# Performance work log

Measured on AMD Instinct MI355X. Metric: run time of the kernel, lower is better.

Reference implementation:

```python
import jax, jax.numpy as jnp
import numpy as np

B, S, H = 2, 2048, 2048
NH, NKV, HD = 16, 4, 128
NEG = -1e9


def rotate_half(x):
    x1, x2 = x[..., : x.shape[-1] // 2], x[..., x.shape[-1] // 2 :]
    return jnp.concatenate((-x2, x1), axis=-1)


def setup_inputs() -> dict:
    key = jax.random.key(0)
    ks = jax.random.split(key, 6)
    hidden_states = jax.random.normal(ks[0], (B, S, H), dtype=jnp.float32)
    # causal additive mask [B, 1, S, S]
    causal = jnp.tril(jnp.ones((S, S), dtype=bool))
    attention_mask = jnp.where(causal, 0.0, NEG).astype(jnp.float32)
    attention_mask = jnp.broadcast_to(attention_mask, (B, 1, S, S))
    # rotary embeddings, base 10000
    inv_freq = 1.0 / (10000.0 ** (np.arange(0, HD, 2, dtype=np.float32) / HD))
    pos = np.arange(S, dtype=np.float32)
    freqs = np.outer(pos, inv_freq)  # [S, HD/2]
    emb = np.concatenate([freqs, freqs], axis=-1)  # [S, HD]
    cos = jnp.broadcast_to(jnp.asarray(np.cos(emb)), (B, S, HD))
    sin = jnp.broadcast_to(jnp.asarray(np.sin(emb)), (B, S, HD))
    sc = 0.02
    Wq = jax.random.normal(ks[1], (H, NH * HD), dtype=jnp.float32) * sc
    Wk = jax.random.normal(ks[2], (H, NKV * HD), dtype=jnp.float32) * sc
    Wv = jax.random.normal(ks[3], (H, NKV * HD), dtype=jnp.float32) * sc
    Wo = jax.random.normal(ks[4], (H, H), dtype=jnp.float32) * sc
    return {"hidden_states": hidden_states, "attention_mask": attention_mask,
            "cos": cos, "sin": sin, "Wq": Wq, "Wk": Wk, "Wv": Wv, "Wo": Wo}


def reference(hidden_states, attention_mask, cos, sin, Wq, Wk, Wv, Wo):
    b, s, _ = hidden_states.shape
    # projections -> [b, heads, s, hd]
    q = (hidden_states @ Wq).reshape(b, s, NH, HD).transpose(0, 2, 1, 3)
    k = (hidden_states @ Wk).reshape(b, s, NKV, HD).transpose(0, 2, 1, 3)
    v = (hidden_states @ Wv).reshape(b, s, NKV, HD).transpose(0, 2, 1, 3)
    # RoPE (cos/sin unsqueezed at dim 1)
    c, sn = cos[:, None], sin[:, None]
    q = q * c + rotate_half(q) * sn
    k = k * c + rotate_half(k) * sn
    # GQA repeat_kv: [b, nkv, s, hd] -> [b, nh, s, hd]
    n_rep = NH // NKV
    k = jnp.repeat(k, n_rep, axis=1)
    v = jnp.repeat(v, n_rep, axis=1)
    scores = jnp.einsum("bhqd,bhkd->bhqk", q, k) / jnp.sqrt(jnp.float32(HD))
    scores = scores + attention_mask
    probs = jax.nn.softmax(scores.astype(jnp.float32), axis=-1).astype(q.dtype)
    out = jnp.einsum("bhqk,bhkd->bhqd", probs, v)
    out = out.transpose(0, 2, 1, 3).reshape(b, s, NH * HD)
    return out @ Wo
```

## Files before the change

### kernel.cpp

```cpp
#include <hip/hip_runtime.h>
#include <hip/hip_bf16.h>

typedef __bf16 bf16;
typedef __bf16 bf16x4 __attribute__((ext_vector_type(4)));
typedef __bf16 bf16x8 __attribute__((ext_vector_type(8)));
typedef float f32x4 __attribute__((ext_vector_type(4)));

__device__ __forceinline__ void gload_lds16(const void* g, void* l) {
  __builtin_amdgcn_global_load_lds((__attribute__((address_space(1))) void*)(g),
                                   (__attribute__((address_space(3))) void*)(l), 16, 0, 0);
}
__device__ __forceinline__ float fexp2(float x) {
  float r;
  asm volatile("v_exp_f32 %0, %1" : "=v"(r) : "v"(x));
  return r;
}

__global__ void k_diag(float* __restrict__ o, float v) { o[threadIdx.x] = v; }

__global__ void k_cvt_bf16(const float* __restrict__ x, bf16* __restrict__ y, int n4) {
  int i = blockIdx.x * blockDim.x + threadIdx.x;
  if (i < n4) {
    float4 v = reinterpret_cast<const float4*>(x)[i];
    bf16x4 o = {(bf16)v.x, (bf16)v.y, (bf16)v.z, (bf16)v.w};
    reinterpret_cast<bf16x4*>(y)[i] = o;
  }
}

__global__ void k_transpose_w(const float* __restrict__ W, bf16* __restrict__ Wt, int K, int N) {
  __shared__ float tile[32][33];
  int kb = blockIdx.x * 32, nb = blockIdx.y * 32;
  int tx = threadIdx.x & 31, ty = threadIdx.x >> 5;
#pragma unroll
  for (int i = 0; i < 32; i += 8)
    tile[ty + i][tx] = W[(size_t)(kb + ty + i) * N + nb + tx];
  __syncthreads();
#pragma unroll
  for (int i = 0; i < 32; i += 8)
    Wt[(size_t)(nb + ty + i) * K + kb + tx] = (bf16)tile[tx][ty + i];
}

__global__ void k_transpose_v(const bf16* __restrict__ KVb, bf16* __restrict__ Vt) {
  __shared__ bf16 tile[32][34];
  constexpr int S = 2048;
  int sb = blockIdx.x * 32, db = blockIdx.y * 32, bh = blockIdx.z;
  int b = bh >> 2, kvh = bh & 3;
  int tx = threadIdx.x & 31, ty = threadIdx.x >> 5;
  const bf16* src = KVb + (size_t)b * S * 1024 + 512 + kvh * 128;
#pragma unroll
  for (int i = 0; i < 32; i += 8)
    tile[ty + i][tx] = src[(size_t)(sb + ty + i) * 1024 + db + tx];
  __syncthreads();
  bf16* dst = Vt + (size_t)bh * 128 * S;
#pragma unroll
  for (int i = 0; i < 32; i += 8)
    dst[(size_t)(db + ty + i) * S + sb + tx] = tile[tx][ty + i];
}

template <typename OT>
__global__ __launch_bounds__(256) void k_gemm(const bf16* __restrict__ A, const bf16* __restrict__ Bt,
                                              OT* __restrict__ C, int M, int N, int Kd) {
  __shared__ __align__(16) bf16 sA[2][128 * 32];
  __shared__ __align__(16) bf16 sB[2][128 * 32];
  const int t = threadIdx.x;
  const int w = t >> 6, l = t & 63;
  const int lr = l & 15, lk = l >> 4;
  const int gx = gridDim.x, nwg = gx * gridDim.y;
  const int flat = blockIdx.y * gx + blockIdx.x;
  const int vid = (flat & 7) * (nwg >> 3) + (flat >> 3);
  const int m0 = (vid % gx) * 128, n0 = (vid / gx) * 128;
  const int wm = (w >> 1) * 64, wn = (w & 1) * 64;
  const bf16* ga = A + (size_t)(m0 + (t >> 2)) * Kd + (t & 3) * 8;
  const bf16* gb = Bt + (size_t)(n0 + (t >> 2)) * Kd + (t & 3) * 8;
  const size_t rowskip = (size_t)64 * Kd;
  auto stage = [&](int k0, int buf) {
    gload_lds16(ga + k0, sA[buf] + w * 512);
    gload_lds16(ga + rowskip + k0, sA[buf] + w * 512 + 2048);
    gload_lds16(gb + k0, sB[buf] + w * 512);
    gload_lds16(gb + rowskip + k0, sB[buf] + w * 512 + 2048);
  };
  f32x4 acc[4][4] = {};
  stage(0, 0);
  __syncthreads();
  int cur = 0;
  for (int k0 = 0; k0 < Kd; k0 += 32) {
    if (k0 + 32 < Kd) stage(k0 + 32, cur ^ 1);
    bf16x8 af[4], bfr[4];
#pragma unroll
    for (int i = 0; i < 4; ++i)
      af[i] = *reinterpret_cast<const bf16x8*>(sA[cur] + (wm + i * 16 + lr) * 32 + lk * 8);
#pragma unroll
    for (int j = 0; j < 4; ++j)
      bfr[j] = *reinterpret_cast<const bf16x8*>(sB[cur] + (wn + j * 16 + lr) * 32 + lk * 8);
#pragma unroll
    for (int i = 0; i < 4; ++i)
#pragma unroll
      for (int j = 0; j < 4; ++j)
        acc[i][j] = __builtin_amdgcn_mfma_f32_16x16x32_bf16(af[i], bfr[j], acc[i][j], 0, 0, 0);
    __syncthreads();
    cur ^= 1;
  }
#pragma unroll
  for (int i = 0; i < 4; ++i)
#pragma unroll
    for (int j = 0; j < 4; ++j)
#pragma unroll
      for (int r = 0; r < 4; ++r) {
        int row = m0 + wm + i * 16 + lk * 4 + r;
        int col = n0 + wn + j * 16 + lr;
        if constexpr (sizeof(OT) == 4)
          C[(size_t)row * N + col] = acc[i][j][r];
        else
          C[(size_t)row * N + col] = (bf16)acc[i][j][r];
      }
}

__global__ void k_rope(bf16* __restrict__ X, const float* __restrict__ cs, const float* __restrict__ sn,
                       int nh, int rowstride, float scale, int total) {
  int idx = blockIdx.x * blockDim.x + threadIdx.x;
  if (idx >= total) return;
  int d = idx & 63;
  int th = idx >> 6;
  int h = th % nh;
  int tok = th / nh;
  size_t base = (size_t)tok * rowstride + h * 128;
  float c = cs[tok * 128 + d], s = sn[tok * 128 + d];
  float x1 = (float)X[base + d];
  float x2 = (float)X[base + d + 64];
  X[base + d] = (bf16)((x1 * c - x2 * s) * scale);
  X[base + d + 64] = (bf16)((x2 * c + x1 * s) * scale);
}

__global__ __launch_bounds__(256) void k_attn(const bf16* __restrict__ Q, const bf16* __restrict__ KV,
                                              const bf16* __restrict__ Vt, bf16* __restrict__ O) {
  constexpr int S = 2048, NH = 16, HD = 128, QSTR = NH * HD, KVSTR = 1024;
  __shared__ __align__(16) bf16 sK[2][64 * 128];
  __shared__ __align__(16) bf16 sV[2][128 * 64];
  __shared__ __align__(16) bf16 sP[4][16][72];
  const int bid = blockIdx.x;
  const int vid = (bid & 7) * 64 + (bid >> 3);
  const int p = vid & 15, bh = vid >> 4;
  const int h = bh & 15, b = bh >> 4;
  const int t = threadIdx.x, w = t >> 6, l = t & 63;
  const int lr = l & 15, lk = l >> 4;
  const int kvh = h >> 2;
  const int swz = (lr & 7) << 4;

  const char* kbase = (const char*)(KV + (size_t)b * S * KVSTR + kvh * HD);
  const int krow_l = w * 16 + (l >> 4);
  const int kcol_l = (l & 15) << 4;
  const char* vtbase = (const char*)(Vt + (size_t)(b * 4 + kvh) * HD * S);
  const int vrow_l = w * 32 + (l >> 3);
  const int vcol_l = (l & 7) << 4;
  char* sKb = (char*)sK;
  char* sVb = (char*)sV;
  auto stage = [&](int kvb, int buf) {
#pragma unroll
    for (int c = 0; c < 4; ++c) {
      const int krow = krow_l + c * 4;
      gload_lds16(kbase + (size_t)(kvb + krow) * 2048 + (kcol_l ^ ((krow & 7) << 4)),
                  sKb + buf * 16384 + (w * 4 + c) * 1024);
      const int vrow = vrow_l + c * 8;
      gload_lds16(vtbase + (size_t)vrow * (S * 2) + kvb * 2 + (vcol_l ^ ((vrow & 7) << 4)),
                  sVb + buf * 16384 + (w * 4 + c) * 1024);
    }
  };

  for (int seg = 0; seg < 2; ++seg) {
    const int qtl = seg ? (31 - p) : p;
    const int qw = qtl * 64 + w * 16;
    const int ntiles = qtl + 1;
    int cur = 0;
    stage(0, 0);
    const bf16* Qp = Q + (size_t)(b * S + qw + lr) * QSTR + h * HD + lk * 8;
    bf16x8 qf[4];
#pragma unroll
    for (int i = 0; i < 4; ++i) qf[i] = *reinterpret_cast<const bf16x8*>(Qp + i * 32);
    f32x4 oacc[8] = {};
    float mrow[4] = {-3e38f, -3e38f, -3e38f, -3e38f};
    float lsum[4] = {0.f, 0.f, 0.f, 0.f};
    __syncthreads();
    for (int tt = 0; tt < ntiles; ++tt) {
      const int kvb = tt * 64;
      if (tt + 1 < ntiles) stage(kvb + 64, cur ^ 1);
      const char* sKc = sKb + cur * 16384;
      const char* sVc = sVb + cur * 16384;
      float pm[4][4];
#pragma unroll
      for (int c = 0; c < 4; ++c) {
        f32x4 s4 = {};
#pragma unroll
        for (int kf = 0; kf < 4; ++kf) {
          bf16x8 kf8 = *reinterpret_cast<const bf16x8*>(
              sKc + (c * 16 + lr) * 256 + (((kf * 64) + (lk << 4)) ^ swz));
          s4 = __builtin_amdgcn_mfma_f32_16x16x32_bf16(qf[kf], kf8, s4, 0, 0, 0);
        }
#pragma unroll
        for (int r = 0; r < 4; ++r) pm[c][r] = s4[r];
      }
      if (tt == ntiles - 1) {
#pragma unroll
        for (int c = 0; c < 4; ++c) {
          const int col = kvb + c * 16 + lr;
#pragma unroll
          for (int r = 0; r < 4; ++r)
            if (col > qw + lk * 4 + r) pm[c][r] = -3e38f;
        }
      }
      float pmax[4];
#pragma unroll
      for (int r = 0; r < 4; ++r)
        pmax[r] = fmaxf(fmaxf(pm[0][r], pm[1][r]), fmaxf(pm[2][r], pm[3][r]));
      bool hi = (pmax[0] > mrow[0] + 8.f) | (pmax[1] > mrow[1] + 8.f) |
                (pmax[2] > mrow[2] + 8.f) | (pmax[3] > mrow[3] + 8.f);
      if (__any(hi)) {
        float mx[4];
#pragma unroll
        for (int r = 0; r < 4; ++r) mx[r] = pmax[r];
#pragma unroll
        for (int off = 1; off < 16; off <<= 1)
#pragma unroll
          for (int r = 0; r < 4; ++r) mx[r] = fmaxf(mx[r], __shfl_xor(mx[r], off));
#pragma unroll
        for (int r = 0; r < 4; ++r) {
          float mn = fmaxf(mrow[r], mx[r]);
          float fac = fexp2(mrow[r] - mn);
          mrow[r] = mn;
          lsum[r] *= fac;
#pragma unroll
          for (int ch = 0; ch < 8; ++ch) oacc[ch][r] *= fac;
        }
      }
#pragma unroll
      for (int c = 0; c < 4; ++c)
#pragma unroll
        for (int r = 0; r < 4; ++r) pm[c][r] = fexp2(pm[c][r] - mrow[r]);
#pragma unroll
      for (int r = 0; r < 4; ++r)
        lsum[r] += (pm[0][r] + pm[1][r]) + (pm[2][r] + pm[3][r]);
#pragma unroll
      for (int c = 0; c < 4; ++c)
#pragma unroll
        for (int r = 0; r < 4; ++r) sP[w][lk * 4 + r][c * 16 + lr] = (bf16)pm[c][r];
      bf16x8 pf0 = *reinterpret_cast<const bf16x8*>(&sP[w][lr][lk * 8]);
      bf16x8 pf1 = *reinterpret_cast<const bf16x8*>(&sP[w][lr][32 + lk * 8]);
#pragma unroll
      for (int ch = 0; ch < 8; ++ch) {
        bf16x8 vf0 = *reinterpret_cast<const bf16x8*>(
            sVc + (ch * 16 + lr) * 128 + ((lk << 4) ^ swz));
        oacc[ch] = __builtin_amdgcn_mfma_f32_16x16x32_bf16(pf0, vf0, oacc[ch], 0, 0, 0);
        bf16x8 vf1 = *reinterpret_cast<const bf16x8*>(
            sVc + (ch * 16 + lr) * 128 + ((64 + (lk << 4)) ^ swz));
        oacc[ch] = __builtin_amdgcn_mfma_f32_16x16x32_bf16(pf1, vf1, oacc[ch], 0, 0, 0);
      }
      __syncthreads();
      cur ^= 1;
    }
#pragma unroll
    for (int off = 1; off < 16; off <<= 1)
#pragma unroll
      for (int r = 0; r < 4; ++r) lsum[r] += __shfl_xor(lsum[r], off);
    float inv[4];
#pragma unroll
    for (int r = 0; r < 4; ++r) inv[r] = 1.0f / lsum[r];
    bf16* Op = O + (size_t)(b * S + qw) * QSTR + h * HD;
#pragma unroll
    for (int ch = 0; ch < 8; ++ch)
#pragma unroll
      for (int r = 0; r < 4; ++r)
        Op[(size_t)(lk * 4 + r) * QSTR + ch * 16 + lr] = (bf16)(oacc[ch][r] * inv[r]);
  }
}

extern "C" void kernel_launch(void* const* d_in, const int* in_sizes, int n_in,
                              void* d_out, int out_size, void* d_ws, size_t ws_size,
                              hipStream_t stream) {
  const float* hs = (const float*)d_in[0];
  const float* cosb = (const float*)d_in[2];
  const float* sinb = (const float*)d_in[3];
  const float* Wq = (const float*)d_in[4];
  const float* Wk = (const float*)d_in[5];
  const float* Wv = (const float*)d_in[6];
  const float* Wo = (const float*)d_in[7];
  float* out = (float*)d_out;

  constexpr int B = 2, S = 2048, H = 2048, NH = 16, NKV = 4, HD = 128;
  constexpr int T = B * S;
  constexpr size_t MB = 1024 * 1024;

  const size_t ws_need = 24 * MB;
  if (ws_size < ws_need) {
    k_diag<<<1, 64, 0, stream>>>(out, 1000.0f + (float)(ws_size / MB));
    return;
  }
  bf16* Xb = (bf16*)d_ws;
  bf16* Wt = (bf16*)((char*)d_ws + 16 * MB);
  bf16* Ob = Xb;
  bf16* Qb = (bf16*)d_out;
  bf16* KVb = (bf16*)((char*)d_out + 16 * MB);
  bf16* Vtb = (bf16*)((char*)d_out + 24 * MB);

  k_cvt_bf16<<<T * H / 4 / 256, 256, 0, stream>>>(hs, Xb, T * H / 4);

  k_transpose_w<<<dim3(H / 32, NH * HD / 32), 256, 0, stream>>>(Wq, Wt, H, NH * HD);
  k_gemm<bf16><<<dim3(T / 128, NH * HD / 128), 256, 0, stream>>>(Xb, Wt, Qb, T, NH * HD, H);

  k_transpose_w<<<dim3(H / 32, NKV * HD / 32), 256, 0, stream>>>(Wk, Wt, H, NKV * HD);
  k_transpose_w<<<dim3(H / 32, NKV * HD / 32), 256, 0, stream>>>(Wv, Wt + (size_t)(NKV * HD) * H, H, NKV * HD);
  k_gemm<bf16><<<dim3(T / 128, 1024 / 128), 256, 0, stream>>>(Xb, Wt, KVb, T, 1024, H);

  k_transpose_v<<<dim3(S / 32, HD / 32, B * NKV), 256, 0, stream>>>(KVb, Vtb);

  const float qscale = 0.12751743f;
  k_rope<<<(T * NH * 64) / 256, 256, 0, stream>>>(Qb, cosb, sinb, NH, NH * HD, qscale, T * NH * 64);
  k_rope<<<(T * NKV * 64) / 256, 256, 0, stream>>>(KVb, cosb, sinb, NKV, 1024, 1.0f, T * NKV * 64);

  k_attn<<<512, 256, 0, stream>>>(Qb, KVb, Vtb, Ob);

  k_transpose_w<<<dim3(H / 32, H / 32), 256, 0, stream>>>(Wo, Wt, H, H);
  k_gemm<float><<<dim3(T / 128, H / 128), 256, 0, stream>>>(Ob, Wt, out, T, H, H);
}
```

Baseline: 255.9 us.

## Rewrite projection GEMMs with 512-thread tiles, K=64 swizzled LDS, and triple-stage pipelining

Replaces the 128x128, 256-thread GEMM with a templated 512-thread kernel that uses 256- or 128-row M tiles and a K step of 64. LDS writes and reads go through an XOR-swizzled layout to avoid bank conflicts. Loads are issued two tiles ahead, using explicit vmcnt waits and raw barriers instead of __syncthreads, and MFMA blocks are wrapped in setprio. The aim is to raise MFMA utilisation and hide global load latency in the Q, KV and output projections, at the cost of larger LDS use, fragile hand-written wait counts and fewer workgroups per GEMM.

```diff
diff --git a/kernel.cpp b/kernel.cpp
--- a/kernel.cpp
+++ b/kernel.cpp
@@ -15,6 +15,7 @@
   asm volatile("v_exp_f32 %0, %1" : "=v"(r) : "v"(x));
   return r;
 }
+#define S_WAITCNT_VM(n) asm volatile("s_waitcnt vmcnt(" #n ")" ::: "memory")
 
 __global__ void k_diag(float* __restrict__ o, float v) { o[threadIdx.x] = v; }
 
@@ -57,57 +58,96 @@
     dst[(size_t)(db + ty + i) * S + sb + tx] = tile[tx][ty + i];
 }
 
-template <typename OT>
-__global__ __launch_bounds__(256) void k_gemm(const bf16* __restrict__ A, const bf16* __restrict__ Bt,
-                                              OT* __restrict__ C, int M, int N, int Kd) {
-  __shared__ __align__(16) bf16 sA[2][128 * 32];
-  __shared__ __align__(16) bf16 sB[2][128 * 32];
-  const int t = threadIdx.x;
-  const int w = t >> 6, l = t & 63;
+template <int BM, typename OT>
+__global__ __launch_bounds__(512) void k_gemm2(const bf16* __restrict__ A, const bf16* __restrict__ Bt,
+                                               OT* __restrict__ C, int N, int Kd) {
+  constexpr int NA = (BM / 16) * 2;
+  constexpr int NB = 16;
+  constexpr int NST = NA + NB;
+  constexpr int NSW = NST / 8;
+  constexpr int WM = BM / 4;
+  constexpr int RG = WM / 16;
+  __shared__ __align__(16) bf16 sAB[2][NST * 512];
+  const int t = threadIdx.x, w = t >> 6, l = t & 63;
   const int lr = l & 15, lk = l >> 4;
-  const int gx = gridDim.x, nwg = gx * gridDim.y;
+  const int gx = gridDim.x;
+  const int nwg = gx * gridDim.y;
   const int flat = blockIdx.y * gx + blockIdx.x;
   const int vid = (flat & 7) * (nwg >> 3) + (flat >> 3);
-  const int m0 = (vid % gx) * 128, n0 = (vid / gx) * 128;
-  const int wm = (w >> 1) * 64, wn = (w & 1) * 64;
-  const bf16* ga = A + (size_t)(m0 + (t >> 2)) * Kd + (t & 3) * 8;
-  const bf16* gb = Bt + (size_t)(n0 + (t >> 2)) * Kd + (t & 3) * 8;
-  const size_t rowskip = (size_t)64 * Kd;
-  auto stage = [&](int k0, int buf) {
-    gload_lds16(ga + k0, sA[buf] + w * 512);
-    gload_lds16(ga + rowskip + k0, sA[buf] + w * 512 + 2048);
-    gload_lds16(gb + k0, sB[buf] + w * 512);
-    gload_lds16(gb + rowskip + k0, sB[buf] + w * 512 + 2048);
+  const int m0 = (vid % gx) * BM, n0 = (vid / gx) * 128;
+  const int wm = w >> 1, wn = w & 1;
+  const int srow = l >> 2;
+  const int lchunk = (l & 3) ^ (((l >> 5) & 1) << 1);
+  const int rdoff = lr * 64 + ((lk * 16) ^ ((lr >> 3) << 5));
+  const int nkt = Kd >> 6;
+  char* lds = (char*)sAB;
+
+  auto stage = [&](int kt, int buf) {
+    const int k0 = kt << 6;
+#pragma unroll
+    for (int u = 0; u < NSW; ++u) {
+      const int s = w * NSW + u;
+      const bf16* src;
+      if (s < NA)
+        src = A + (size_t)(m0 + (s >> 1) * 16 + srow) * Kd + k0 + (s & 1) * 32 + lchunk * 8;
+      else
+        src = Bt + (size_t)(n0 + ((s - NA) >> 1) * 16 + srow) * Kd + k0 + ((s - NA) & 1) * 32 + lchunk * 8;
+      gload_lds16(src, lds + buf * (NST * 1024) + s * 1024);
+    }
   };
-  f32x4 acc[4][4] = {};
+
+  f32x4 acc[RG][4] = {};
   stage(0, 0);
-  __syncthreads();
-  int cur = 0;
-  for (int k0 = 0; k0 < Kd; k0 += 32) {
-    if (k0 + 32 < Kd) stage(k0 + 32, cur ^ 1);
-    bf16x8 af[4], bfr[4];
-#pragma unroll
-    for (int i = 0; i < 4; ++i)
-      af[i] = *reinterpret_cast<const bf16x8*>(sA[cur] + (wm + i * 16 + lr) * 32 + lk * 8);
+  stage(1, 1);
+  if constexpr (NSW == 6) S_WAITCNT_VM(6); else S_WAITCNT_VM(4);
+  __builtin_amdgcn_s_barrier();
+  int c = 0;
+  for (int kt = 0; kt < nkt; ++kt) {
+    __builtin_amdgcn_sched_barrier(0);
+    const char* base = lds + c * (NST * 1024);
+    bf16x8 af[RG][2], bfr[4][2];
+#pragma unroll
+    for (int i = 0; i < RG; ++i)
+#pragma unroll
+      for (int kk = 0; kk < 2; ++kk)
+        af[i][kk] = *reinterpret_cast<const bf16x8*>(base + ((wm * RG + i) * 2 + kk) * 1024 + rdoff);
 #pragma unroll
     for (int j = 0; j < 4; ++j)
-      bfr[j] = *reinterpret_cast<const bf16x8*>(sB[cur] + (wn + j * 16 + lr) * 32 + lk * 8);
-#pragma unroll
-    for (int i = 0; i < 4; ++i)
-#pragma unroll
-      for (int j = 0; j < 4; ++j)
-        acc[i][j] = __builtin_amdgcn_mfma_f32_16x16x32_bf16(af[i], bfr[j], acc[i][j], 0, 0, 0);
-    __syncthreads();
-    cur ^= 1;
+#pragma unroll
+      for (int kk = 0; kk < 2; ++kk)
+        bfr[j][kk] = *reinterpret_cast<const bf16x8*>(base + (NA + (wn * 4 + j) * 2 + kk) * 1024 + rdoff);
+    __builtin_amdgcn_s_setprio(1);
+#pragma unroll
+    for (int i = 0; i < RG; ++i)
+#pragma unroll
+      for (int j = 0; j < 4; ++j) {
+        acc[i][j] = __builtin_amdgcn_mfma_f32_16x16x32_bf16(af[i][0], bfr[j][0], acc[i][j], 0, 0, 0);
+        acc[i][j] = __builtin_amdgcn_mfma_f32_16x16x32_bf16(af[i][1], bfr[j][1], acc[i][j], 0, 0, 0);
+      }
+    __builtin_amdgcn_s_setprio(0);
+    __builtin_amdgcn_sched_barrier(0);
+    asm volatile("" ::: "memory");
+    __builtin_amdgcn_s_barrier();
+    if (kt + 2 < nkt) stage(kt + 2, c);
+    if (kt + 1 < nkt) {
+      if (kt + 2 < nkt) {
+        if constexpr (NSW == 6) S_WAITCNT_VM(6); else S_WAITCNT_VM(4);
+      } else {
+        S_WAITCNT_VM(0);
+      }
+      asm volatile("" ::: "memory");
+      __builtin_amdgcn_s_barrier();
+    }
+    c ^= 1;
   }
 #pragma unroll
-  for (int i = 0; i < 4; ++i)
+  for (int i = 0; i < RG; ++i)
 #pragma unroll
     for (int j = 0; j < 4; ++j)
 #pragma unroll
       for (int r = 0; r < 4; ++r) {
-        int row = m0 + wm + i * 16 + lk * 4 + r;
-        int col = n0 + wn + j * 16 + lr;
+        int row = m0 + wm * WM + i * 16 + lk * 4 + r;
+        int col = n0 + wn * 64 + j * 16 + lr;
         if constexpr (sizeof(OT) == 4)
           C[(size_t)row * N + col] = acc[i][j][r];
         else
@@ -303,11 +343,11 @@
   k_cvt_bf16<<<T * H / 4 / 256, 256, 0, stream>>>(hs, Xb, T * H / 4);
 
   k_transpose_w<<<dim3(H / 32, NH * HD / 32), 256, 0, stream>>>(Wq, Wt, H, NH * HD);
-  k_gemm<bf16><<<dim3(T / 128, NH * HD / 128), 256, 0, stream>>>(Xb, Wt, Qb, T, NH * HD, H);
+  k_gemm2<256, bf16><<<dim3(16, 16), 512, 0, stream>>>(Xb, Wt, Qb, NH * HD, H);
 
   k_transpose_w<<<dim3(H / 32, NKV * HD / 32), 256, 0, stream>>>(Wk, Wt, H, NKV * HD);
   k_transpose_w<<<dim3(H / 32, NKV * HD / 32), 256, 0, stream>>>(Wv, Wt + (size_t)(NKV * HD) * H, H, NKV * HD);
-  k_gemm<bf16><<<dim3(T / 128, 1024 / 128), 256, 0, stream>>>(Xb, Wt, KVb, T, 1024, H);
+  k_gemm2<128, bf16><<<dim3(32, 8), 512, 0, stream>>>(Xb, Wt, KVb, 1024, H);
 
   k_transpose_v<<<dim3(S / 32, HD / 32, B * NKV), 256, 0, stream>>>(KVb, Vtb);
 
@@ -318,5 +358,5 @@
   k_attn<<<512, 256, 0, stream>>>(Qb, KVb, Vtb, Ob);
 
   k_transpose_w<<<dim3(H / 32, H / 32), 256, 0, stream>>>(Wo, Wt, H, H);
-  k_gemm<float><<<dim3(T / 128, H / 128), 256, 0, stream>>>(Ob, Wt, out, T, H, H);
-}
+  k_gemm2<256, float><<<dim3(16, 16), 512, 0, stream>>>(Ob, Wt, out, H, H);
+}
```

Result: faster. 226.0 us (-11.7%).

## Fuse QKV projections into one 256x256-tile GEMM with swizzled fine-grained pipeline

Applied to the files above, without the earlier changes.

Replaces the 128x128 two-stage GEMM with a 512-thread kernel computing 256x256 tiles over K-steps of 64. It adds XOR-swizzled LDS layouts, per-quarter vmcnt waits with raw barriers, and raised MFMA priority so loads overlap compute. The Q and KV projections are merged into a single launch writing a packed 3072-wide QKV buffer, and the attention, RoPE and V-transpose kernels are re-strided to read it. The aim is more operand reuse per tile and fewer launches. The cost is a larger LDS footprint (128KB) and fewer workgroups (192 and 128), which may underfill the GPU's CUs.

```diff
diff --git a/kernel.cpp b/kernel.cpp
--- a/kernel.cpp
+++ b/kernel.cpp
@@ -15,6 +15,7 @@
   asm volatile("v_exp_f32 %0, %1" : "=v"(r) : "v"(x));
   return r;
 }
+#define S_WAITCNT_VM(n) asm volatile("s_waitcnt vmcnt(" #n ")" ::: "memory")
 
 __global__ void k_diag(float* __restrict__ o, float v) { o[threadIdx.x] = v; }
 
@@ -40,16 +41,16 @@
     Wt[(size_t)(nb + ty + i) * K + kb + tx] = (bf16)tile[tx][ty + i];
 }
 
-__global__ void k_transpose_v(const bf16* __restrict__ KVb, bf16* __restrict__ Vt) {
+__global__ void k_transpose_v(const bf16* __restrict__ Cq, bf16* __restrict__ Vt) {
   __shared__ bf16 tile[32][34];
-  constexpr int S = 2048;
+  constexpr int S = 2048, CSTR = 3072;
   int sb = blockIdx.x * 32, db = blockIdx.y * 32, bh = blockIdx.z;
   int b = bh >> 2, kvh = bh & 3;
   int tx = threadIdx.x & 31, ty = threadIdx.x >> 5;
-  const bf16* src = KVb + (size_t)b * S * 1024 + 512 + kvh * 128;
+  const bf16* src = Cq + (size_t)b * S * CSTR + 2560 + kvh * 128;
 #pragma unroll
   for (int i = 0; i < 32; i += 8)
-    tile[ty + i][tx] = src[(size_t)(sb + ty + i) * 1024 + db + tx];
+    tile[ty + i][tx] = src[(size_t)(sb + ty + i) * CSTR + db + tx];
   __syncthreads();
   bf16* dst = Vt + (size_t)bh * 128 * S;
 #pragma unroll
@@ -58,60 +59,87 @@
 }
 
 template <typename OT>
-__global__ __launch_bounds__(256) void k_gemm(const bf16* __restrict__ A, const bf16* __restrict__ Bt,
-                                              OT* __restrict__ C, int M, int N, int Kd) {
-  __shared__ __align__(16) bf16 sA[2][128 * 32];
-  __shared__ __align__(16) bf16 sB[2][128 * 32];
-  const int t = threadIdx.x;
-  const int w = t >> 6, l = t & 63;
+__global__ __launch_bounds__(512) void k_gemm3(const bf16* __restrict__ A,
+                                               const bf16* __restrict__ B0,
+                                               const bf16* __restrict__ B1, int nsplit,
+                                               OT* __restrict__ C, int Ncols, int Kd) {
+  __shared__ __align__(16) bf16 lds_[65536];
+  char* lds = (char*)lds_;
+  const int t = threadIdx.x, w = t >> 6, l = t & 63;
   const int lr = l & 15, lk = l >> 4;
   const int gx = gridDim.x, nwg = gx * gridDim.y;
   const int flat = blockIdx.y * gx + blockIdx.x;
   const int vid = (flat & 7) * (nwg >> 3) + (flat >> 3);
-  const int m0 = (vid % gx) * 128, n0 = (vid / gx) * 128;
-  const int wm = (w >> 1) * 64, wn = (w & 1) * 64;
-  const bf16* ga = A + (size_t)(m0 + (t >> 2)) * Kd + (t & 3) * 8;
-  const bf16* gb = Bt + (size_t)(n0 + (t >> 2)) * Kd + (t & 3) * 8;
-  const size_t rowskip = (size_t)64 * Kd;
-  auto stage = [&](int k0, int buf) {
-    gload_lds16(ga + k0, sA[buf] + w * 512);
-    gload_lds16(ga + rowskip + k0, sA[buf] + w * 512 + 2048);
-    gload_lds16(gb + k0, sB[buf] + w * 512);
-    gload_lds16(gb + rowskip + k0, sB[buf] + w * 512 + 2048);
+  const int m0 = (vid % gx) * 256, n0 = (vid / gx) * 256;
+  const int wm = w >> 2, wn = w & 3;
+  const bf16* Bt = (n0 < nsplit) ? B0 + (size_t)n0 * Kd : B1 + (size_t)(n0 - nsplit) * Kd;
+  const int nkt = Kd >> 6;
+  const int srow = l >> 2;
+  const int lch = (l & 3) ^ ((srow + (srow >> 2)) & 3);
+  auto stA = [&](int tile, int unit) {
+    if (tile >= nkt) return;
+    const bf16* s = A + (size_t)(m0 + unit * 64 + (w >> 1) * 16 + srow) * Kd +
+                    (tile << 6) + (w & 1) * 32 + lch * 8;
+    gload_lds16(s, lds + (tile & 1) * 32768 + unit * 8192 + w * 1024);
   };
-  f32x4 acc[4][4] = {};
-  stage(0, 0);
-  __syncthreads();
-  int cur = 0;
-  for (int k0 = 0; k0 < Kd; k0 += 32) {
-    if (k0 + 32 < Kd) stage(k0 + 32, cur ^ 1);
-    bf16x8 af[4], bfr[4];
-#pragma unroll
-    for (int i = 0; i < 4; ++i)
-      af[i] = *reinterpret_cast<const bf16x8*>(sA[cur] + (wm + i * 16 + lr) * 32 + lk * 8);
+  auto stB = [&](int tile, int grp) {
+    if (tile >= nkt) return;
+    const bf16* s = Bt + (size_t)((w >> 1) * 64 + grp * 16 + srow) * Kd +
+                    (tile << 6) + (w & 1) * 32 + lch * 8;
+    gload_lds16(s, lds + 65536 + (tile & 1) * 32768 + grp * 8192 + w * 1024);
+  };
+  const int rdoff = lr * 64 + ((lk ^ ((lr + (lr >> 2)) & 3)) << 4);
+
+  f32x4 acc[8][4] = {};
+  stA(0, 0); stA(0, 1); stA(0, 2); stA(0, 3);
+  stB(0, 0);
+  stA(1, 0); stB(0, 1); stA(1, 1); stB(0, 2); stA(1, 2); stB(0, 3);
+
+  for (int kt = 0; kt < nkt; ++kt) {
+    const int buf = kt & 1;
+    const char* Ab = lds + buf * 32768;
+    const char* Bb = lds + 65536 + buf * 32768;
+    bf16x8 af[8][2];
+#pragma unroll
+    for (int p = 0; p < 4; ++p) {
+      if (kt + 1 < nkt) { S_WAITCNT_VM(6); } else { S_WAITCNT_VM(0); }
+      __builtin_amdgcn_sched_barrier(0);
+      __builtin_amdgcn_s_barrier();
+      __builtin_amdgcn_sched_barrier(0);
+      if (p == 0) stA(kt + 1, 3); else stA(kt + 2, p - 1);
+      stB(kt + 1, p);
+      if (p == 0) {
+#pragma unroll
+        for (int i = 0; i < 8; ++i) {
+          const char* ub = Ab + (wm * 2 + (i >> 2)) * 8192 + (i & 3) * 2048;
+          af[i][0] = *reinterpret_cast<const bf16x8*>(ub + rdoff);
+          af[i][1] = *reinterpret_cast<const bf16x8*>(ub + 1024 + rdoff);
+        }
+      }
+      bf16x8 b0 = *reinterpret_cast<const bf16x8*>(Bb + p * 8192 + wn * 2048 + rdoff);
+      bf16x8 b1 = *reinterpret_cast<const bf16x8*>(Bb + p * 8192 + wn * 2048 + 1024 + rdoff);
+      __builtin_amdgcn_s_setprio(1);
+#pragma unroll
+      for (int i = 0; i < 8; ++i) {
+        acc[i][p] = __builtin_amdgcn_mfma_f32_16x16x32_bf16(af[i][0], b0, acc[i][p], 0, 0, 0);
+        acc[i][p] = __builtin_amdgcn_mfma_f32_16x16x32_bf16(af[i][1], b1, acc[i][p], 0, 0, 0);
+      }
+      __builtin_amdgcn_s_setprio(0);
+      __builtin_amdgcn_sched_barrier(0);
+    }
+  }
+#pragma unroll
+  for (int i = 0; i < 8; ++i)
 #pragma unroll
     for (int j = 0; j < 4; ++j)
-      bfr[j] = *reinterpret_cast<const bf16x8*>(sB[cur] + (wn + j * 16 + lr) * 32 + lk * 8);
-#pragma unroll
-    for (int i = 0; i < 4; ++i)
-#pragma unroll
-      for (int j = 0; j < 4; ++j)
-        acc[i][j] = __builtin_amdgcn_mfma_f32_16x16x32_bf16(af[i], bfr[j], acc[i][j], 0, 0, 0);
-    __syncthreads();
-    cur ^= 1;
-  }
-#pragma unroll
-  for (int i = 0; i < 4; ++i)
-#pragma unroll
-    for (int j = 0; j < 4; ++j)
 #pragma unroll
       for (int r = 0; r < 4; ++r) {
-        int row = m0 + wm + i * 16 + lk * 4 + r;
-        int col = n0 + wn + j * 16 + lr;
+        int row = m0 + wm * 128 + i * 16 + lk * 4 + r;
+        int col = n0 + wn * 64 + j * 16 + lr;
         if constexpr (sizeof(OT) == 4)
-          C[(size_t)row * N + col] = acc[i][j][r];
+          C[(size_t)row * Ncols + col] = acc[i][j][r];
         else
-          C[(size_t)row * N + col] = (bf16)acc[i][j][r];
+          C[(size_t)row * Ncols + col] = (bf16)acc[i][j][r];
       }
 }
 
@@ -133,7 +161,7 @@
 
 __global__ __launch_bounds__(256) void k_attn(const bf16* __restrict__ Q, const bf16* __restrict__ KV,
                                               const bf16* __restrict__ Vt, bf16* __restrict__ O) {
-  constexpr int S = 2048, NH = 16, HD = 128, QSTR = NH * HD, KVSTR = 1024;
+  constexpr int S = 2048, HD = 128, QSTR = 3072, OSTR = 2048;
   __shared__ __align__(16) bf16 sK[2][64 * 128];
   __shared__ __align__(16) bf16 sV[2][128 * 64];
   __shared__ __align__(16) bf16 sP[4][16][72];
@@ -146,7 +174,7 @@
   const int kvh = h >> 2;
   const int swz = (lr & 7) << 4;
 
-  const char* kbase = (const char*)(KV + (size_t)b * S * KVSTR + kvh * HD);
+  const char* kbase = (const char*)(KV + (size_t)b * S * QSTR + kvh * HD);
   const int krow_l = w * 16 + (l >> 4);
   const int kcol_l = (l & 15) << 4;
   const char* vtbase = (const char*)(Vt + (size_t)(b * 4 + kvh) * HD * S);
@@ -158,7 +186,7 @@
 #pragma unroll
     for (int c = 0; c < 4; ++c) {
       const int krow = krow_l + c * 4;
-      gload_lds16(kbase + (size_t)(kvb + krow) * 2048 + (kcol_l ^ ((krow & 7) << 4)),
+      gload_lds16(kbase + (size_t)(kvb + krow) * (QSTR * 2) + (kcol_l ^ ((krow & 7) << 4)),
                   sKb + buf * 16384 + (w * 4 + c) * 1024);
       const int vrow = vrow_l + c * 8;
       gload_lds16(vtbase + (size_t)vrow * (S * 2) + kvb * 2 + (vcol_l ^ ((vrow & 7) << 4)),
@@ -263,12 +291,12 @@
     float inv[4];
 #pragma unroll
     for (int r = 0; r < 4; ++r) inv[r] = 1.0f / lsum[r];
-    bf16* Op = O + (size_t)(b * S + qw) * QSTR + h * HD;
+    bf16* Op = O + (size_t)(b * S + qw) * OSTR + h * HD;
 #pragma unroll
     for (int ch = 0; ch < 8; ++ch)
 #pragma unroll
       for (int r = 0; r < 4; ++r)
-        Op[(size_t)(lk * 4 + r) * QSTR + ch * 16 + lr] = (bf16)(oacc[ch][r] * inv[r]);
+        Op[(size_t)(lk * 4 + r) * OSTR + ch * 16 + lr] = (bf16)(oacc[ch][r] * inv[r]);
   }
 }
 
@@ -294,29 +322,28 @@
     return;
   }
   bf16* Xb = (bf16*)d_ws;
-  bf16* Wt = (bf16*)((char*)d_ws + 16 * MB);
+  bf16* WtQ = (bf16*)((char*)d_ws + 16 * MB);
   bf16* Ob = Xb;
-  bf16* Qb = (bf16*)d_out;
-  bf16* KVb = (bf16*)((char*)d_out + 16 * MB);
+  bf16* Cqkv = (bf16*)d_out;
   bf16* Vtb = (bf16*)((char*)d_out + 24 * MB);
+  bf16* WtKV = (bf16*)((char*)d_out + 28 * MB);
 
   k_cvt_bf16<<<T * H / 4 / 256, 256, 0, stream>>>(hs, Xb, T * H / 4);
 
-  k_transpose_w<<<dim3(H / 32, NH * HD / 32), 256, 0, stream>>>(Wq, Wt, H, NH * HD);
-  k_gemm<bf16><<<dim3(T / 128, NH * HD / 128), 256, 0, stream>>>(Xb, Wt, Qb, T, NH * HD, H);
-
-  k_transpose_w<<<dim3(H / 32, NKV * HD / 32), 256, 0, stream>>>(Wk, Wt, H, NKV * HD);
-  k_transpose_w<<<dim3(H / 32, NKV * HD / 32), 256, 0, stream>>>(Wv, Wt + (size_t)(NKV * HD) * H, H, NKV * HD);
-  k_gemm<bf16><<<dim3(T / 128, 1024 / 128), 256, 0, stream>>>(Xb, Wt, KVb, T, 1024, H);
-
-  k_transpose_v<<<dim3(S / 32, HD / 32, B * NKV), 256, 0, stream>>>(KVb, Vtb);
+  k_transpose_w<<<dim3(H / 32, H / 32), 256, 0, stream>>>(Wq, WtQ, H, H);
+  k_transpose_w<<<dim3(H / 32, (NKV * HD) / 32), 256, 0, stream>>>(Wk, WtKV, H, NKV * HD);
+  k_transpose_w<<<dim3(H / 32, (NKV * HD) / 32), 256, 0, stream>>>(Wv, WtKV + (size_t)(NKV * HD) * H, H, NKV * HD);
+
+  k_gemm3<bf16><<<dim3(16, 12), 512, 0, stream>>>(Xb, WtQ, WtKV, 2048, Cqkv, 3072, H);
+
+  k_transpose_v<<<dim3(S / 32, HD / 32, B * NKV), 256, 0, stream>>>(Cqkv, Vtb);
 
   const float qscale = 0.12751743f;
-  k_rope<<<(T * NH * 64) / 256, 256, 0, stream>>>(Qb, cosb, sinb, NH, NH * HD, qscale, T * NH * 64);
-  k_rope<<<(T * NKV * 64) / 256, 256, 0, stream>>>(KVb, cosb, sinb, NKV, 1024, 1.0f, T * NKV * 64);
-
-  k_attn<<<512, 256, 0, stream>>>(Qb, KVb, Vtb, Ob);
-
-  k_transpose_w<<<dim3(H / 32, H / 32), 256, 0, stream>>>(Wo, Wt, H, H);
-  k_gemm<float><<<dim3(T / 128, H / 128), 256, 0, stream>>>(Ob, Wt, out, T, H, H);
-}
+  k_rope<<<(T * NH * 64) / 256, 256, 0, stream>>>(Cqkv, cosb, sinb, NH, 3072, qscale, T * NH * 64);
+  k_rope<<<(T * NKV * 64) / 256, 256, 0, stream>>>(Cqkv + 2048, cosb, sinb, NKV, 3072, 1.0f, T * NKV * 64);
+
+  k_attn<<<512, 256, 0, stream>>>(Cqkv, Cqkv + 2048, Vtb, Ob);
+
+  k_transpose_w<<<dim3(H / 32, H / 32), 256, 0, stream>>>(Wo, WtQ, H, H);
+  k_gemm3<float><<<dim3(16, 8), 512, 0, stream>>>(Ob, WtQ, WtQ, 1 << 30, out, H, H);
+}
```

New measurement: 249.2 us. -2.6%, faster.
